# Performance work log

Hardware: AMD Instinct MI355X
Metric: run time of the kernel (lower is better)

The kernel has to match this reference:

```python
import jax, jax.numpy as jnp
import numpy as np

N_NODES = 50000
N_EDGES = 600000
D = 128            # out_feats
N_ETYPES = 4
N_STEPS = 5


def setup_inputs() -> dict:
    key = jax.random.key(0)
    ks = jax.random.split(key, 10)
    h = jax.random.normal(ks[0], (N_NODES, D), dtype=jnp.float32)
    src = jax.random.randint(ks[1], (N_EDGES,), 0, N_NODES)
    dst = jax.random.randint(ks[2], (N_EDGES,), 0, N_NODES)
    # rel_type values are 1..n_etypes in the original module
    etypes = jax.random.randint(ks[3], (N_EDGES,), 1, N_ETYPES + 1)
    s = 1.0 / np.sqrt(D)
    # per-edge-type Linear(out_feats, out_feats): y = x @ W.T + b
    W_lin = jax.random.normal(ks[4], (N_ETYPES, D, D), dtype=jnp.float32) * s
    b_lin = jnp.zeros((N_ETYPES, D), dtype=jnp.float32)
    # GRUCell params (torch layout: rows ordered r, z, n)
    w_ih = jax.random.uniform(ks[5], (3 * D, D), minval=-s, maxval=s, dtype=jnp.float32)
    w_hh = jax.random.uniform(ks[6], (3 * D, D), minval=-s, maxval=s, dtype=jnp.float32)
    b_ih = jax.random.uniform(ks[7], (3 * D,), minval=-s, maxval=s, dtype=jnp.float32)
    b_hh = jax.random.uniform(ks[8], (3 * D,), minval=-s, maxval=s, dtype=jnp.float32)
    return {"h": h, "src": src, "dst": dst, "etypes": etypes,
            "W_lin": W_lin, "b_lin": b_lin,
            "w_ih": w_ih, "w_hh": w_hh, "b_ih": b_ih, "b_hh": b_hh}


def _gru_cell(a, h, w_ih, w_hh, b_ih, b_hh):
    gi = a @ w_ih.T + b_ih          # [N, 3D]
    gh = h @ w_hh.T + b_hh          # [N, 3D]
    i_r, i_z, i_n = jnp.split(gi, 3, axis=-1)
    h_r, h_z, h_n = jnp.split(gh, 3, axis=-1)
    r = jax.nn.sigmoid(i_r + h_r)
    z = jax.nn.sigmoid(i_z + h_z)
    n = jnp.tanh(i_n + r * h_n)
    return (1.0 - z) * n + z * h


def reference(h, src, dst, etypes, W_lin, b_lin, w_ih, w_hh, b_ih, b_hh):
    N = h.shape[0]
    et = etypes - 1                 # 0-based edge type index
    for _ in range(N_STEPS):
        # per-type node transforms: t[k] = h @ W_lin[k].T + b_lin[k]  -> [K, N, D]
        t = jnp.einsum('nd,kfd->knf', h, W_lin) + b_lin[:, None, :]
        msg = t[et, src]            # gather per-edge transformed source feats [E, D]
        a = jax.ops.segment_sum(msg, dst, num_segments=N)  # scatter-sum aggregation
        h = _gru_cell(a, h, w_ih, w_hh, b_ih, b_hh)
    return h
```

## Files before the change

kernel.cpp:

```cpp
#include <hip/hip_runtime.h>
#include <hip/hip_bf16.h>
#include <cstdint>
#include <cstddef>

#define N_NODES 50000
#define N_EDGES 600000
#define DF 128
#define N_ETYPES 4
#define N_STEPS 5
#define SCAN_NB 196
#define GRU_TILES 3125
#define GRU_BLOCKS 256
#define LIN_BLOCKS 256
#define TSTRIDE 136
#define FILL_CHUNKS 2344
#define FILL_RANGE (N_NODES / 8)

typedef _Float16 f16x8 __attribute__((ext_vector_type(8)));
typedef _Float16 f16x4 __attribute__((ext_vector_type(4)));
typedef float f32x4 __attribute__((ext_vector_type(4)));

__device__ __forceinline__ float sigmoid_fast(float x) {
    return 1.0f / (1.0f + __expf(-x));
}
__device__ __forceinline__ float tanh_fast(float x) {
    return 1.0f - 2.0f / (__expf(2.0f * x) + 1.0f);
}


__global__ __launch_bounds__(256) void k_setup(
    const float* __restrict__ Wl, const float* __restrict__ wih,
    const float* __restrict__ whh, const float* __restrict__ h,
    const int* __restrict__ dst,
    _Float16* __restrict__ Wl_h, _Float16* __restrict__ Bc,
    _Float16* __restrict__ hh, int* __restrict__ deg) {
    int i = blockIdx.x * 256 + threadIdx.x;
    if (i < N_ETYPES * DF * DF * 3 / 2) {
        if (i < N_ETYPES * DF * DF) Wl_h[i] = (_Float16)Wl[i];
        int row = i >> 8;
        int k = i & 255;
        float v = (k < 128) ? wih[row * 128 + k] : whh[row * 128 + (k - 128)];
        Bc[i] = (_Float16)v;
    }
    if (i < N_NODES * DF / 4) {
        float4 v = ((const float4*)h)[i];
        f16x4 o;
        o.x = (_Float16)v.x; o.y = (_Float16)v.y;
        o.z = (_Float16)v.z; o.w = (_Float16)v.w;
        ((f16x4*)hh)[i] = o;
    }
    if (i < N_EDGES) atomicAdd(&deg[dst[i]], 1);
}

__global__ __launch_bounds__(256) void k_part(
    const int* __restrict__ deg, int* __restrict__ part, int N) {
    __shared__ int s[256];
    int t = threadIdx.x, i = blockIdx.x * 256 + t;
    s[t] = (i < N) ? deg[i] : 0;
    __syncthreads();
    for (int off = 128; off > 0; off >>= 1) {
        if (t < off) s[t] += s[t + off];
        __syncthreads();
    }
    if (t == 0) part[blockIdx.x] = s[0];
}

__global__ __launch_bounds__(256) void k_scan1(int* __restrict__ part, int nb) {
    __shared__ int s[256];
    int t = threadIdx.x;
    int v = (t < nb) ? part[t] : 0;
    s[t] = v;
    __syncthreads();
    for (int off = 1; off < 256; off <<= 1) {
        int u = (t >= off) ? s[t - off] : 0;
        __syncthreads();
        s[t] += u;
        __syncthreads();
    }
    if (t < nb) part[t] = s[t] - v;
}

__global__ __launch_bounds__(256) void k_row(
    const int* __restrict__ deg, const int* __restrict__ part,
    int* __restrict__ row_start, int* __restrict__ cursor, int N) {
    __shared__ int s[256];
    int t = threadIdx.x, i = blockIdx.x * 256 + t;
    int d = (i < N) ? deg[i] : 0;
    s[t] = d;
    __syncthreads();
    for (int off = 1; off < 256; off <<= 1) {
        int u = (t >= off) ? s[t - off] : 0;
        __syncthreads();
        s[t] += u;
        __syncthreads();
    }
    int rs = part[blockIdx.x] + s[t] - d;
    if (i < N) {
        row_start[i] = rs;
        cursor[i] = rs;
        if (i == N - 1) row_start[N] = rs + d;
    }
}

__global__ __launch_bounds__(256) void k_fill(
    const int* __restrict__ src, const int* __restrict__ dst,
    const int* __restrict__ ety, int* __restrict__ cursor,
    int* __restrict__ csr, int E) {
    const int range = blockIdx.x & 7;
    const int chunk = blockIdx.x >> 3;
    const int e = chunk * 256 + threadIdx.x;
    const int lo = range * FILL_RANGE;
    const int hi = lo + FILL_RANGE;
    if (e < E) {
        int d = dst[e];
        if (d >= lo && d < hi) {
            int slot = atomicAdd(&cursor[d], 1);
            csr[slot] = src[e] | ((ety[e] - 1) << 16);
        }
    }
}


__global__ __launch_bounds__(1024) void k_lin(
    const _Float16* __restrict__ hh, const _Float16* __restrict__ Wl,
    const float* __restrict__ b_lin, _Float16* __restrict__ t_out, int N) {
    __shared__ _Float16 O[2][N_ETYPES * 16 * TSTRIDE];
    __shared__ __align__(16) char Ast[4][4096];
    const int wave = threadIdx.x >> 6, lane = threadIdx.x & 63;
    const int col16 = lane & 15, quad = lane >> 4;
    const int g = wave >> 2;
    const int s = wave & 3;

    f16x8 b[2][4];
#pragma unroll
    for (int ct = 0; ct < 2; ct++) {
        const _Float16* bp = Wl + (size_t)g * DF * DF
                           + (size_t)(s * 32 + ct * 16 + col16) * DF + quad * 8;
#pragma unroll
        for (int kt = 0; kt < 4; kt++) b[ct][kt] = *(const f16x8*)(bp + kt * 32);
    }
    const float bias0 = b_lin[g * DF + s * 32 + col16];
    const float bias1 = b_lin[g * DF + s * 32 + 16 + col16];

    const int olocal = (wave & 3) * 1024 + lane * 16;
    const int oswl = olocal ^ (((olocal >> 8) & 7) << 4);
    const int abase = col16 * 256 + quad * 16;
    const int axor = (col16 & 7) << 4;

    auto STAGE = [&](int iter) {
        if (wave < 4) {
            int tt = blockIdx.x + iter * LIN_BLOCKS;
            if (tt >= GRU_TILES) tt = GRU_TILES - 1;
            const char* gp = (const char*)hh + (size_t)tt * 4096 + oswl;
            char* lp = &Ast[iter & 3][(wave & 3) * 1024];
            __builtin_amdgcn_global_load_lds(
                (const __attribute__((address_space(1))) void*)gp,
                (__attribute__((address_space(3))) void*)lp, 16, 0, 0);
        }
    };

    const int ek = threadIdx.x >> 8;
    const int erow = (threadIdx.x & 255) >> 4;
    const int ec8 = threadIdx.x & 15;

    STAGE(0);
    STAGE(1);
    asm volatile("s_waitcnt vmcnt(1)" ::: "memory");
    __builtin_amdgcn_s_barrier();
    __builtin_amdgcn_sched_barrier(0);

    int it = 0;
    for (int tile = blockIdx.x; tile < GRU_TILES; tile += LIN_BLOCKS, ++it) {
        const int r0 = tile * 16;
        STAGE(it + 2);

        const char* As = (const char*)Ast[it & 3];
        _Float16* Ob = O[it & 1];

        f16x8 A[4];
#pragma unroll
        for (int kt = 0; kt < 4; kt++) {
            int off = (abase + kt * 64) ^ axor;
            A[kt] = *(const f16x8*)(As + off);
        }

        f32x4 acc0 = {0.f, 0.f, 0.f, 0.f}, acc1 = {0.f, 0.f, 0.f, 0.f};
#pragma unroll
        for (int kt = 0; kt < 4; kt++) {
            acc0 = __builtin_amdgcn_mfma_f32_16x16x32_f16(A[kt], b[0][kt], acc0, 0, 0, 0);
            acc1 = __builtin_amdgcn_mfma_f32_16x16x32_f16(A[kt], b[1][kt], acc1, 0, 0, 0);
        }

        _Float16* Og = Ob + g * (16 * TSTRIDE);
#pragma unroll
        for (int i = 0; i < 4; i++) {
            Og[(quad * 4 + i) * TSTRIDE + s * 32 + col16] = (_Float16)(acc0[i] + bias0);
            Og[(quad * 4 + i) * TSTRIDE + s * 32 + 16 + col16] = (_Float16)(acc1[i] + bias1);
        }

        asm volatile("s_waitcnt vmcnt(1) lgkmcnt(0)" ::: "memory");
        __builtin_amdgcn_s_barrier();
        __builtin_amdgcn_sched_barrier(0);

        f16x8 v = *(const f16x8*)&Ob[ek * (16 * TSTRIDE) + erow * TSTRIDE + ec8 * 8];
        *(f16x8*)(t_out + ((size_t)ek * N + (r0 + erow)) * DF + ec8 * 8) = v;
    }
    asm volatile("s_waitcnt vmcnt(0)" ::: "memory");
}

__global__ __launch_bounds__(256) void k_agg(
    const _Float16* __restrict__ t, const int* __restrict__ row_start,
    const int* __restrict__ csr, _Float16* __restrict__ ah, int N) {
    const int wave = threadIdx.x >> 6, lane = threadIdx.x & 63;
    const int g4 = lane >> 4;
    const int c8 = lane & 15;
    const int n = blockIdx.x * 4 + wave;
    const int beg = row_start[n], end = row_start[n + 1];
    float acc[8] = {0.f, 0.f, 0.f, 0.f, 0.f, 0.f, 0.f, 0.f};
    for (int e = beg; e < end; e += 16) {
        int i0 = e + g4, i1 = e + 4 + g4, i2 = e + 8 + g4, i3 = e + 12 + g4;
        float m0 = (i0 < end) ? 1.0f : 0.0f;
        float m1 = (i1 < end) ? 1.0f : 0.0f;
        float m2 = (i2 < end) ? 1.0f : 0.0f;
        float m3 = (i3 < end) ? 1.0f : 0.0f;
        int j0 = (i0 < end) ? i0 : end - 1;
        int j1 = (i1 < end) ? i1 : end - 1;
        int j2 = (i2 < end) ? i2 : end - 1;
        int j3 = (i3 < end) ? i3 : end - 1;
        int p0 = csr[j0], p1 = csr[j1], p2 = csr[j2], p3 = csr[j3];
        f16x8 x0 = *(const f16x8*)(t + ((((size_t)(p0 >> 16)) * N + (p0 & 0xFFFF)) << 7) + c8 * 8);
        f16x8 x1 = *(const f16x8*)(t + ((((size_t)(p1 >> 16)) * N + (p1 & 0xFFFF)) << 7) + c8 * 8);
        f16x8 x2 = *(const f16x8*)(t + ((((size_t)(p2 >> 16)) * N + (p2 & 0xFFFF)) << 7) + c8 * 8);
        f16x8 x3 = *(const f16x8*)(t + ((((size_t)(p3 >> 16)) * N + (p3 & 0xFFFF)) << 7) + c8 * 8);
#pragma unroll
        for (int j = 0; j < 8; j++) acc[j] += m0 * (float)x0[j];
#pragma unroll
        for (int j = 0; j < 8; j++) acc[j] += m1 * (float)x1[j];
#pragma unroll
        for (int j = 0; j < 8; j++) acc[j] += m2 * (float)x2[j];
#pragma unroll
        for (int j = 0; j < 8; j++) acc[j] += m3 * (float)x3[j];
    }
#pragma unroll
    for (int j = 0; j < 8; j++) {
        acc[j] += __shfl_xor(acc[j], 32, 64);
        acc[j] += __shfl_xor(acc[j], 16, 64);
    }
    if (lane < 16) {
        f16x8 o;
#pragma unroll
        for (int j = 0; j < 8; j++) o[j] = (_Float16)acc[j];
        *(f16x8*)(ah + ((size_t)n << 7) + c8 * 8) = o;
    }
}

__global__ __launch_bounds__(512) void k_gru(
    const _Float16* __restrict__ ah, const _Float16* __restrict__ hh,
    const _Float16* __restrict__ Bc, const float* __restrict__ b_ih,
    const float* __restrict__ b_hh, _Float16* __restrict__ hh_next,
    float* __restrict__ out_f32) {
    __shared__ __align__(16) char Ast[4][8192];
    __shared__ _Float16 Tw[8][16][20];
    const int wave = threadIdx.x >> 6, lane = threadIdx.x & 63;
    const int col16 = lane & 15, quad = lane >> 4;
    const int c = wave * 16 + col16;

    f16x8 br[8], bz[8], bi[4], bh[4];
    {
        const _Float16* Br = Bc + ((size_t)c << 8);
        const _Float16* Bz = Bc + ((size_t)(128 + c) << 8);
        const _Float16* Bn = Bc + ((size_t)(256 + c) << 8);
#pragma unroll
        for (int kt = 0; kt < 8; kt++) {
            br[kt] = *(const f16x8*)(Br + kt * 32 + quad * 8);
            bz[kt] = *(const f16x8*)(Bz + kt * 32 + quad * 8);
        }
#pragma unroll
        for (int kt = 0; kt < 4; kt++) {
            bi[kt] = *(const f16x8*)(Bn + kt * 32 + quad * 8);
            bh[kt] = *(const f16x8*)(Bn + 128 + kt * 32 + quad * 8);
        }
    }
    const float bir = b_ih[c] + b_hh[c];
    const float biz = b_ih[128 + c] + b_hh[128 + c];
    const float bin_ = b_ih[256 + c];
    const float bhn_ = b_hh[256 + c];

    const int olocal = (wave & 3) * 1024 + lane * 16;
    const int oswl = olocal ^ (((olocal >> 8) & 7) << 4);
    const char* sbase = (wave < 4) ? (const char*)ah : (const char*)hh;
    const int abase = col16 * 256 + quad * 16;
    const int axor = (col16 & 7) << 4;

    auto STAGE = [&](int iter) {
        int tt = blockIdx.x + iter * GRU_BLOCKS;
        if (tt >= GRU_TILES) tt = GRU_TILES - 1;
        const char* gp = sbase + (size_t)tt * 4096 + oswl;
        char* lp = &Ast[iter & 3][wave * 1024];
        __builtin_amdgcn_global_load_lds(
            (const __attribute__((address_space(1))) void*)gp,
            (__attribute__((address_space(3))) void*)lp, 16, 0, 0);
    };

    STAGE(0);
    STAGE(1);
    asm volatile("s_waitcnt vmcnt(1)" ::: "memory");
    __builtin_amdgcn_s_barrier();
    __builtin_amdgcn_sched_barrier(0);

    int it = 0;
    for (int tile = blockIdx.x; tile < GRU_TILES; tile += GRU_BLOCKS, ++it) {
        const int r0 = tile * 16;
        STAGE(it + 2);

        const char* As = (const char*)Ast[it & 3];

        f16x8 A[8];
#pragma unroll
        for (int kt = 0; kt < 8; kt++) {
            int off = ((kt & 4) << 10) + abase + (kt & 3) * 64;
            off ^= axor;
            A[kt] = *(const f16x8*)(As + off);
        }

        f32x4 ar = {0.f, 0.f, 0.f, 0.f}, az = {0.f, 0.f, 0.f, 0.f};
        f32x4 ai = {0.f, 0.f, 0.f, 0.f}, an = {0.f, 0.f, 0.f, 0.f};
#pragma unroll
        for (int kt = 0; kt < 8; kt++) {
            ar = __builtin_amdgcn_mfma_f32_16x16x32_f16(A[kt], br[kt], ar, 0, 0, 0);
            az = __builtin_amdgcn_mfma_f32_16x16x32_f16(A[kt], bz[kt], az, 0, 0, 0);
        }
#pragma unroll
        for (int kt = 0; kt < 4; kt++) {
            ai = __builtin_amdgcn_mfma_f32_16x16x32_f16(A[kt], bi[kt], ai, 0, 0, 0);
            an = __builtin_amdgcn_mfma_f32_16x16x32_f16(A[4 + kt], bh[kt], an, 0, 0, 0);
        }

#pragma unroll
        for (int i = 0; i < 4; i++) {
            int row = quad * 4 + i;
            int hoff = (4096 + row * 256 + c * 2) ^ ((row & 7) << 4);
            float hprev = (float)*(const _Float16*)(As + hoff);
            float r = sigmoid_fast(ar[i] + bir);
            float z = sigmoid_fast(az[i] + biz);
            float nn = tanh_fast(ai[i] + bin_ + r * (an[i] + bhn_));
            float hv = (1.f - z) * nn + z * hprev;
            if (out_f32) {
                out_f32[((size_t)(r0 + row) << 7) + c] = hv;
            } else {
                Tw[wave][row][col16] = (_Float16)hv;
            }
        }
        if (!out_f32) {
            int row = lane >> 2, ch = lane & 3;
            f16x4 v = *(const f16x4*)&Tw[wave][row][ch * 4];
            *(f16x4*)(hh_next + ((size_t)(r0 + row) << 7) + wave * 16 + ch * 4) = v;
        }

        asm volatile("s_waitcnt vmcnt(1) lgkmcnt(0)" ::: "memory");
        __builtin_amdgcn_s_barrier();
        __builtin_amdgcn_sched_barrier(0);
    }
    asm volatile("s_waitcnt vmcnt(0)" ::: "memory");
}


extern "C" void kernel_launch(void* const* d_in, const int* in_sizes, int n_in,
                              void* d_out, int out_size, void* d_ws, size_t ws_size,
                              hipStream_t stream) {
    const float* h0    = (const float*)d_in[0];
    const int*   src   = (const int*)d_in[1];
    const int*   dst   = (const int*)d_in[2];
    const int*   ety   = (const int*)d_in[3];
    const float* W_lin = (const float*)d_in[4];
    const float* b_lin = (const float*)d_in[5];
    const float* w_ih  = (const float*)d_in[6];
    const float* w_hh  = (const float*)d_in[7];
    const float* b_ih  = (const float*)d_in[8];
    const float* b_hh  = (const float*)d_in[9];
    float* hout = (float*)d_out;

    char* p = (char*)d_ws;
    auto alloc = [&](size_t bytes) -> char* {
        char* r = p;
        p += (bytes + 255) & ~(size_t)255;
        return r;
    };
    _Float16* h_a    = (_Float16*)alloc((size_t)N_NODES * DF * 2);
    _Float16* h_b    = (_Float16*)alloc((size_t)N_NODES * DF * 2);
    _Float16* a_half = (_Float16*)alloc((size_t)N_NODES * DF * 2);
    _Float16* t_half = (_Float16*)alloc((size_t)N_ETYPES * N_NODES * DF * 2);
    _Float16* Wl_h   = (_Float16*)alloc((size_t)N_ETYPES * DF * DF * 2);
    _Float16* Bc     = (_Float16*)alloc((size_t)3 * DF * 2 * DF * 2);
    int* deg       = (int*)alloc((size_t)N_NODES * 4);
    int* row_start = (int*)alloc((size_t)(N_NODES + 1) * 4);
    int* cursor    = (int*)alloc((size_t)N_NODES * 4);
    int* csr       = (int*)alloc((size_t)N_EDGES * 4);
    int* part      = (int*)alloc((size_t)SCAN_NB * 4);

    hipMemsetAsync(deg, 0, (size_t)N_NODES * 4, stream);
    k_setup<<<(N_NODES * DF / 4 + 255) / 256, 256, 0, stream>>>(
        W_lin, w_ih, w_hh, h0, dst, Wl_h, Bc, h_a, deg);
    k_part<<<SCAN_NB, 256, 0, stream>>>(deg, part, N_NODES);
    k_scan1<<<1, 256, 0, stream>>>(part, SCAN_NB);
    k_row<<<SCAN_NB, 256, 0, stream>>>(deg, part, row_start, cursor, N_NODES);
    k_fill<<<FILL_CHUNKS * 8, 256, 0, stream>>>(src, dst, ety, cursor, csr, N_EDGES);

    _Float16* hc = h_a;
    _Float16* hn = h_b;
    for (int s = 0; s < N_STEPS; s++) {
        k_lin<<<LIN_BLOCKS, 1024, 0, stream>>>(hc, Wl_h, b_lin, t_half, N_NODES);
        k_agg<<<N_NODES / 4, 256, 0, stream>>>(t_half, row_start, csr, a_half, N_NODES);
        float* of = (s == N_STEPS - 1) ? hout : nullptr;
        k_gru<<<GRU_BLOCKS, 512, 0, stream>>>(a_half, hc, Bc, b_ih, b_hh, hn, of);
        _Float16* tmp = hc; hc = hn; hn = tmp;
    }
}
```

Measured before the change: 522.3 us.

## Fuse next-step per-type linear transform into GRU kernel epilogue

The GRU kernel now stages each new hidden tile in shared memory and immediately applies the four per-edge-type linear transforms with MFMA, writing the next step's transformed features directly. The standalone linear kernel runs once before the loop instead of every step, saving four launches and a re-read of the hidden state. In exchange the GRU kernel holds extra weight registers and shared memory and adds a barrier per tile, which may reduce occupancy.

After: 514.1 us. Within noise of the previous version (-1.6%).

```diff
diff --git a/kernel.cpp b/kernel.cpp
--- a/kernel.cpp
+++ b/kernel.cpp
@@ -13,6 +13,7 @@
 #define GRU_BLOCKS 256
 #define LIN_BLOCKS 256
 #define TSTRIDE 136
+#define OSTR 76
 #define FILL_CHUNKS 2344
 #define FILL_RANGE (N_NODES / 8)
 
@@ -254,13 +255,15 @@
     }
 }
 
-__global__ __launch_bounds__(512) void k_gru(
+__global__ __launch_bounds__(512) void k_grulin(
     const _Float16* __restrict__ ah, const _Float16* __restrict__ hh,
     const _Float16* __restrict__ Bc, const float* __restrict__ b_ih,
-    const float* __restrict__ b_hh, _Float16* __restrict__ hh_next,
-    float* __restrict__ out_f32) {
+    const float* __restrict__ b_hh, const _Float16* __restrict__ Wl,
+    const float* __restrict__ b_lin, _Float16* __restrict__ hh_next,
+    _Float16* __restrict__ t_out, float* __restrict__ out_f32, int N) {
     __shared__ __align__(16) char Ast[4][8192];
-    __shared__ _Float16 Tw[8][16][20];
+    __shared__ __align__(16) char Hn[2][4096];
+    __shared__ _Float16 Ow[8][16 * OSTR];
     const int wave = threadIdx.x >> 6, lane = threadIdx.x & 63;
     const int col16 = lane & 15, quad = lane >> 4;
     const int c = wave * 16 + col16;
@@ -285,6 +288,19 @@
     const float biz = b_ih[128 + c] + b_hh[128 + c];
     const float bin_ = b_ih[256 + c];
     const float bhn_ = b_hh[256 + c];
+
+    const int et = wave >> 1;
+    const int ch64 = (wave & 1) * 64;
+    f16x8 wl[4][4];
+    float blv[4];
+#pragma unroll
+    for (int ct = 0; ct < 4; ct++) {
+        const _Float16* wp = Wl + (size_t)et * DF * DF
+                           + (size_t)(ch64 + ct * 16 + col16) * DF + quad * 8;
+#pragma unroll
+        for (int kt = 0; kt < 4; kt++) wl[ct][kt] = *(const f16x8*)(wp + kt * 32);
+        blv[ct] = b_lin[et * DF + ch64 + ct * 16 + col16];
+    }
 
     const int olocal = (wave & 3) * 1024 + lane * 16;
     const int oswl = olocal ^ (((olocal >> 8) & 7) << 4);
@@ -336,6 +352,7 @@
             an = __builtin_amdgcn_mfma_f32_16x16x32_f16(A[4 + kt], bh[kt], an, 0, 0, 0);
         }
 
+        char* Hb = Hn[it & 1];
 #pragma unroll
         for (int i = 0; i < 4; i++) {
             int row = quad * 4 + i;
@@ -348,18 +365,51 @@
             if (out_f32) {
                 out_f32[((size_t)(r0 + row) << 7) + c] = hv;
             } else {
-                Tw[wave][row][col16] = (_Float16)hv;
+                *(_Float16*)(Hb + ((row * 256 + c * 2) ^ ((row & 7) << 4))) = (_Float16)hv;
             }
         }
-        if (!out_f32) {
-            int row = lane >> 2, ch = lane & 3;
-            f16x4 v = *(const f16x4*)&Tw[wave][row][ch * 4];
-            *(f16x4*)(hh_next + ((size_t)(r0 + row) << 7) + wave * 16 + ch * 4) = v;
+
+        if (t_out) {
+            asm volatile("s_waitcnt lgkmcnt(0)" ::: "memory");
+            __builtin_amdgcn_s_barrier();
+            __builtin_amdgcn_sched_barrier(0);
+
+            f16x8 A2[4];
+#pragma unroll
+            for (int kt = 0; kt < 4; kt++) {
+                int off = (col16 * 256 + kt * 64 + quad * 16) ^ ((col16 & 7) << 4);
+                A2[kt] = *(const f16x8*)(Hb + off);
+            }
+#pragma unroll
+            for (int ct = 0; ct < 4; ct++) {
+                f32x4 acc = {0.f, 0.f, 0.f, 0.f};
+#pragma unroll
+                for (int kt = 0; kt < 4; kt++)
+                    acc = __builtin_amdgcn_mfma_f32_16x16x32_f16(A2[kt], wl[ct][kt], acc, 0, 0, 0);
+#pragma unroll
+                for (int i = 0; i < 4; i++)
+                    Ow[wave][(quad * 4 + i) * OSTR + ct * 16 + col16] = (_Float16)(acc[i] + blv[ct]);
+            }
         }
 
         asm volatile("s_waitcnt vmcnt(1) lgkmcnt(0)" ::: "memory");
         __builtin_amdgcn_s_barrier();
         __builtin_amdgcn_sched_barrier(0);
+
+        if (!out_f32) {
+            int hrow = threadIdx.x >> 5, hch = threadIdx.x & 31;
+            f16x4 hv4 = *(const f16x4*)(Hb + ((hrow * 256 + hch * 8) ^ ((hrow & 7) << 4)));
+            *(f16x4*)(hh_next + ((size_t)(r0 + hrow) << 7) + hch * 4) = hv4;
+        }
+        if (t_out) {
+#pragma unroll
+            for (int j = 0; j < 2; j++) {
+                int chunk = lane + 64 * j;
+                int trow = chunk >> 3, c8 = chunk & 7;
+                f16x8 v = *(const f16x8*)&Ow[wave][trow * OSTR + c8 * 8];
+                *(f16x8*)(t_out + ((size_t)et * N + (r0 + trow)) * DF + ch64 + c8 * 8) = v;
+            }
+        }
     }
     asm volatile("s_waitcnt vmcnt(0)" ::: "memory");
 }
@@ -408,11 +458,13 @@
 
     _Float16* hc = h_a;
     _Float16* hn = h_b;
+    k_lin<<<LIN_BLOCKS, 1024, 0, stream>>>(hc, Wl_h, b_lin, t_half, N_NODES);
     for (int s = 0; s < N_STEPS; s++) {
-        k_lin<<<LIN_BLOCKS, 1024, 0, stream>>>(hc, Wl_h, b_lin, t_half, N_NODES);
         k_agg<<<N_NODES / 4, 256, 0, stream>>>(t_half, row_start, csr, a_half, N_NODES);
-        float* of = (s == N_STEPS - 1) ? hout : nullptr;
-        k_gru<<<GRU_BLOCKS, 512, 0, stream>>>(a_half, hc, Bc, b_ih, b_hh, hn, of);
+        const bool last = (s == N_STEPS - 1);
+        k_grulin<<<GRU_BLOCKS, 512, 0, stream>>>(
+            a_half, hc, Bc, b_ih, b_hh, Wl_h, b_lin, hn,
+            last ? nullptr : t_half, last ? hout : nullptr, N_NODES);
         _Float16* tmp = hc; hc = hn; hn = tmp;
     }
 }
```
